# Kernel tuning notes

Hardware: AMD Instinct MI355X
Metric: run time of the kernel (lower is better)

The kernel has to match this reference:

```python
import jax, jax.numpy as jnp
import numpy as np
import math

# Mamba2Simple(d_model=192, d_state=128, d_conv=4, expand=4, headdim=32, chunk_size=256)
D_MODEL = 192
D_STATE = 128
D_CONV = 4
EXPAND = 4
HEADDIM = 32
D_INNER = EXPAND * D_MODEL                      # 768
NHEADS = D_INNER // HEADDIM                     # 24
CONV_DIM = D_INNER + 2 * D_STATE                # 1024 (ngroups=1)
D_IN_PROJ = 2 * D_INNER + 2 * D_STATE + NHEADS  # 1816
SEQ_PAD = 256                                   # forward pads dim-2 to 256
NUM_CLASS = 100
FEATURE_DIM = HEADDIM * D_STATE                 # 4096, classifier input


def make_pe(max_len, d_model):
    # TemporalPositionalEncoding buffer (sin/cos), added over the T axis.
    position = np.arange(max_len)[:, None].astype(np.float32)
    div_term = np.exp(np.arange(0, d_model, 2).astype(np.float32) * -(math.log(10000.0) / d_model))
    pe = np.zeros((max_len, d_model), np.float32)
    pe[:, 0::2] = np.sin(position * div_term)
    pe[:, 1::2] = np.cos(position * div_term)
    return jnp.asarray(pe)  # (max_len, d_model)


def setup_inputs() -> dict:
    key = jax.random.key(0)
    ks = jax.random.split(key, 8)
    B, T, S, D = 16, 8, 129, D_MODEL
    inputs = jax.random.normal(ks[0], (B, T, S, D), jnp.float32)
    in_proj_w = jax.random.normal(ks[1], (D_IN_PROJ, D_MODEL), jnp.float32) / np.sqrt(D_MODEL)
    conv_w = jax.random.normal(ks[2], (CONV_DIM, D_CONV), jnp.float32) / np.sqrt(D_CONV)
    conv_b = jax.random.normal(ks[3], (CONV_DIM,), jnp.float32) * 0.1
    # dt_bias = softplus^{-1}(dt) with dt ~ U[1e-3, 0.1] (Mamba2 init convention)
    dt0 = jax.random.uniform(ks[4], (NHEADS,), jnp.float32, 1e-3, 0.1)
    dt_bias = jnp.log(jnp.expm1(dt0))
    A_log = jnp.log(jax.random.uniform(ks[5], (NHEADS,), jnp.float32, 1.0, 16.0))
    cls_w = jax.random.normal(ks[6], (NUM_CLASS, FEATURE_DIM), jnp.float32) / np.sqrt(FEATURE_DIM)
    cls_b = jnp.zeros((NUM_CLASS,), jnp.float32)
    return dict(inputs=inputs, in_proj_w=in_proj_w, conv_w=conv_w, conv_b=conv_b,
                dt_bias=dt_bias, A_log=A_log, cls_w=cls_w, cls_b=cls_b)


def _mamba_final_state(u, in_proj_w, conv_w, conv_b, dt_bias, A_log):
    # u: (B, L, D_MODEL). Only the SSM final state is consumed downstream
    # (the module does `_, final_state = self.mamba(...)`), so the z / C / D /
    # RMSNormGated / out_proj branches, which never touch the state, are skipped.
    B_, L, _ = u.shape
    W = in_proj_w[D_INNER:, :]                              # rows for xBC (1024) + dt (24)
    proj = jnp.einsum('bld,ed->ble', u, W)                  # (B, L, 1048)
    xBC, dt_raw = proj[..., :CONV_DIM], proj[..., CONV_DIM:]
    # causal depthwise conv1d (kernel D_CONV) + SiLU
    xpad = jnp.pad(xBC, ((0, 0), (D_CONV - 1, 0), (0, 0)))
    conv = conv_b + sum(xpad[:, k:k + L, :] * conv_w[:, k] for k in range(D_CONV))
    xBC = jax.nn.silu(conv)
    x = xBC[..., :D_INNER].reshape(B_, L, NHEADS, HEADDIM)  # (B, L, H, P)
    Bmat = xBC[..., D_INNER:D_INNER + D_STATE]              # (B, L, N), ngroups=1
    dt = jax.nn.softplus(dt_raw + dt_bias)                  # (B, L, H)
    A = -jnp.exp(A_log)                                     # (H,), negative
    # Recurrence: h_t = exp(dt_t*A) * h_{t-1} + dt_t * x_t (outer) B_t.
    # Final state in closed form via exclusive suffix products of exp(dt*A):
    logdA = dt * A                                          # (B, L, H), <= 0
    csum = jnp.cumsum(logdA, axis=1)
    suffix = jnp.exp(csum[:, -1:, :] - csum)                # prod_{s>t} exp(dt_s*A)
    w = suffix * dt                                         # (B, L, H)
    return jnp.einsum('blh,blhp,bln->bhpn', w, x, Bmat)     # (B, H, P, N)


def reference(inputs, in_proj_w, conv_w, conv_b, dt_bias, A_log, cls_w, cls_b):
    # Dropout layers are identity in eval mode.
    B_, T, S, D = inputs.shape
    x = inputs[:, :, 1:, :]                                 # drop first sub-seq element
    pad = SEQ_PAD - x.shape[2]
    if pad > 0:
        x = jnp.pad(x, ((0, 0), (0, 0), (0, pad), (0, 0)))
    pe = make_pe(T, D)
    x = x + pe[None, :, None, :]                            # pe broadcast over batch & sub-seq
    preds = []
    for t in range(T):                                      # module re-runs scan on each suffix
        xt = x[:, t:, :, :].reshape(B_, -1, D)              # (B, (T-t)*256, D)
        h = _mamba_final_state(xt, in_proj_w, conv_w, conv_b, dt_bias, A_log)
        agg = h.sum(axis=1).reshape(B_, FEATURE_DIM)        # sum over heads -> (B, P*N)
        preds.append(agg @ cls_w.T + cls_b)
    return jnp.stack(preds, axis=1)                         # (B, T, NUM_CLASS)
```

## Files before the change

### kernel.cpp

```cpp
#include <hip/hip_runtime.h>
#include <math.h>

#define BATCH 16
#define TWIN 8
#define SEQIN 129
#define DMODEL 192
#define GLEN 2048
#define NH 24
#define HD 32
#define DS 128
#define NCC 896
#define MTOT (BATCH*GLEN)
#define NVALID (BATCH*TWIN*128)
#define PADK 104

typedef __attribute__((ext_vector_type(8))) short bf16x8;
typedef __attribute__((ext_vector_type(4))) float f32x4;

__device__ __forceinline__ float softplus_f(float x){
  return x > 20.f ? x : log1pf(expf(x));
}
__device__ __forceinline__ float silu_f(float x){
  return x / (1.f + __expf(-x));
}
__device__ __forceinline__ unsigned short tobf16(float f){
  union { float f; unsigned u; } v; v.f = f;
  unsigned r = v.u + 0x7FFF + ((v.u >> 16) & 1);
  return (unsigned short)(r >> 16);
}
__device__ __forceinline__ float frombf16(unsigned short u){
  union { unsigned u; float f; } v; v.u = ((unsigned)u) << 16; return v.f;
}
__device__ __forceinline__ bf16x8 pack8(float4 a, float4 b){
  bf16x8 r;
  r[0]=(short)tobf16(a.x); r[1]=(short)tobf16(a.y);
  r[2]=(short)tobf16(a.z); r[3]=(short)tobf16(a.w);
  r[4]=(short)tobf16(b.x); r[5]=(short)tobf16(b.y);
  r[6]=(short)tobf16(b.z); r[7]=(short)tobf16(b.w);
  return r;
}

__global__ __launch_bounds__(256) void k_build(const float* __restrict__ in,
    const float* __restrict__ inw, unsigned short* __restrict__ inh,
    unsigned short* __restrict__ wh, float* __restrict__ ptab,
    float* __restrict__ dtraw){
  __shared__ float smem[2048];
  int bx = blockIdx.x;
  int tid = threadIdx.x;
  if (bx < 768){
    int idx = (bx*256 + tid)*16;
    int v = idx / DMODEL;
    int d = idx - v*DMODEL;
    int bt = v >> 7, s = v & 127;
    const float* src = in + ((size_t)bt*SEQIN + s + 1)*DMODEL + d;
    float4 a0 = *(const float4*)src;
    float4 a1 = *(const float4*)(src+4);
    float4 a2 = *(const float4*)(src+8);
    float4 a3 = *(const float4*)(src+12);
    *(bf16x8*)&inh[idx]   = pack8(a0, a1);
    *(bf16x8*)&inh[idx+8] = pack8(a2, a3);
  } else if (bx < 852){
    int idx = ((bx-768)*256 + tid)*8;
    const float* src = inw + (size_t)768*DMODEL + idx;
    float4 a = *(const float4*)src;
    float4 b = *(const float4*)(src+4);
    *(bf16x8*)&wh[idx] = pack8(a, b);
  } else if (bx < 916){
    float* pe = smem;
    int pb = bx - 852;
    int t = pb >> 3, eslice = pb & 7;
    if (tid < DMODEL){
      int d = tid;
      float div = expf(-(float)(d & ~1) * (logf(10000.f)/(float)DMODEL));
      float ang = (float)t * div;
      pe[d] = (d & 1) ? cosf(ang) : sinf(ang);
    }
    __syncthreads();
    int e0 = eslice*115;
    int e1 = min(920, e0 + 115);
    for (int e = e0 + tid; e < e1; e += 256){
      int row = (e < 896) ? (768 + e) : (1792 + (e - 896));
      const float* wr = inw + (size_t)row*DMODEL;
      float s = 0.f;
      #pragma unroll 4
      for (int d = 0; d < DMODEL; d++)
        s += pe[d] * wr[d];
      ptab[t*920 + e] = s;
    }
  } else {
    float* As = smem;
    float* Bs = smem + 1024;
    int idx = bx - 916;
    int m0 = idx*64;
    int bt = m0 >> 7, srow = m0 & 127;
    int ty = tid >> 4, tx = tid & 15;
    int lr = tid >> 2, lq = tid & 3;
    float acc[4][4] = {};
    for (int k0 = 0; k0 < DMODEL; k0 += 16){
      float4 av = *(const float4*)(in + ((size_t)bt*SEQIN + srow + 1 + lr)*DMODEL + k0 + lq*4);
      As[(lq*4+0)*64+lr] = av.x; As[(lq*4+1)*64+lr] = av.y;
      As[(lq*4+2)*64+lr] = av.z; As[(lq*4+3)*64+lr] = av.w;
      float4 bv = make_float4(0.f,0.f,0.f,0.f);
      if (lr < NH) bv = *(const float4*)(inw + (size_t)(1792+lr)*DMODEL + k0 + lq*4);
      Bs[(lq*4+0)*64+lr] = bv.x; Bs[(lq*4+1)*64+lr] = bv.y;
      Bs[(lq*4+2)*64+lr] = bv.z; Bs[(lq*4+3)*64+lr] = bv.w;
      __syncthreads();
      #pragma unroll
      for (int kk = 0; kk < 16; kk++){
        float4 a = *(const float4*)&As[kk*64 + ty*4];
        float4 bq = *(const float4*)&Bs[kk*64 + tx*4];
        float avr[4] = {a.x, a.y, a.z, a.w};
        float bvr[4] = {bq.x, bq.y, bq.z, bq.w};
        #pragma unroll
        for (int i=0;i<4;i++)
          #pragma unroll
          for (int j=0;j<4;j++)
            acc[i][j] += avr[i]*bvr[j];
      }
      __syncthreads();
    }
    #pragma unroll
    for (int i=0;i<4;i++){
      int m = m0 + ty*4 + i;
      #pragma unroll
      for (int j=0;j<4;j++){
        int n = tx*4 + j;
        if (n < NH) dtraw[(size_t)m*NH + n] = acc[i][j];
      }
    }
  }
}

__global__ __launch_bounds__(256) void k_gemmall(const unsigned short* __restrict__ inh,
    const unsigned short* __restrict__ wh, const float* __restrict__ ptab,
    const float* __restrict__ dtraw, const float* __restrict__ dt_bias,
    const float* __restrict__ A_log, unsigned short* __restrict__ projh,
    float* __restrict__ wbuf, float* __restrict__ wsum){
  __shared__ char smem[53248];
  int bx = blockIdx.x;
  int tid = threadIdx.x;
  if (bx < 896){
    unsigned short* As = (unsigned short*)smem;
    unsigned short* Bs = As + 128*PADK;
    int mt = bx & 127;
    int n0 = (bx >> 7)*128;
    int t = mt & 7;
    size_t msrc = (size_t)mt*128;
    size_t mdst = (size_t)(mt >> 3)*GLEN + (size_t)t*256;
    int wid = tid >> 6, lane = tid & 63;
    int wm = (wid >> 1)*64, wn = (wid & 1)*64;
    int quad = lane >> 4, lm = lane & 15;
    int sr = tid >> 2, sq = tid & 3;
    f32x4 acc[4][4];
    #pragma unroll
    for (int i=0;i<4;i++)
      #pragma unroll
      for (int j=0;j<4;j++) acc[i][j] = (f32x4){0.f,0.f,0.f,0.f};
    for (int k0 = 0; k0 < DMODEL; k0 += 96){
      #pragma unroll
      for (int kk = 0; kk < 96; kk += 32){
        #pragma unroll
        for (int half=0; half<2; half++){
          int r = sr + half*64;
          *(bf16x8*)&As[r*PADK + kk + sq*8] =
            *(const bf16x8*)&inh[(msrc + r)*DMODEL + k0 + kk + sq*8];
          *(bf16x8*)&Bs[r*PADK + kk + sq*8] =
            *(const bf16x8*)&wh[(size_t)(n0+r)*DMODEL + k0 + kk + sq*8];
        }
      }
      __syncthreads();
      #pragma unroll
      for (int kk = 0; kk < 3; kk++){
        bf16x8 aF[4], bF[4];
        #pragma unroll
        for (int i=0;i<4;i++){
          aF[i] = *(const bf16x8*)&As[(wm + i*16 + lm)*PADK + kk*32 + quad*8];
          bF[i] = *(const bf16x8*)&Bs[(wn + i*16 + lm)*PADK + kk*32 + quad*8];
        }
        #pragma unroll
        for (int i=0;i<4;i++)
          #pragma unroll
          for (int j=0;j<4;j++)
            acc[i][j] = __builtin_amdgcn_mfma_f32_16x16x32_bf16(aF[i], bF[j], acc[i][j], 0,0,0);
      }
      __syncthreads();
    }
    float ptn[4];
    #pragma unroll
    for (int j=0;j<4;j++) ptn[j] = ptab[t*920 + n0 + wn + lm + j*16];
    #pragma unroll
    for (int i=0;i<4;i++){
      #pragma unroll
      for (int r=0;r<4;r++){
        int m = wm + i*16 + quad*4 + r;
        unsigned short* dst = projh + (mdst + m)*NCC + n0 + wn + lm;
        #pragma unroll
        for (int j=0;j<4;j++)
          dst[j*16] = tobf16(acc[i][j][r] + ptn[j]);
      }
    }
    {
      int r = tid >> 5;
      int c4 = (tid & 31)*4;
      float4 pv = *(const float4*)&ptab[t*920 + n0 + c4];
      ushort4 v;
      v.x = tobf16(pv.x); v.y = tobf16(pv.y);
      v.z = tobf16(pv.z); v.w = tobf16(pv.w);
      *(ushort4*)&projh[(mdst + 128 + r)*NCC + n0 + c4] = v;
    }
  } else {
    float* wtot = (float*)smem;
    float* sred = (float*)smem + 4;
    int idx = bx - 896;
    int h = idx % NH, b = idx / NH;
    int lane = tid & 63, wid = tid >> 6;
    int tw = tid >> 5, q = tid & 31;
    float dtb = dt_bias[h];
    float negA = -expf(A_log[h]);
    float off = ptab[tw*920 + 896 + h] + dtb;
    float dtv[8], pre[8];
    float run = 0.f;
    if (q < 16){
      size_t rb = ((size_t)(b*TWIN + tw)*128 + q*8)*NH + h;
      #pragma unroll
      for (int i=0;i<8;i++){
        float dt = softplus_f(dtraw[rb + (size_t)i*NH] + off);
        run += dt * negA;
        dtv[i] = dt; pre[i] = run;
      }
    } else {
      float dt = softplus_f(off);
      #pragma unroll
      for (int i=0;i<8;i++){
        run += dt * negA;
        dtv[i] = dt; pre[i] = run;
      }
    }
    float v = run;
    #pragma unroll
    for (int o=1; o<64; o<<=1){
      float u = __shfl_up(v, o, 64);
      if (lane >= o) v += u;
    }
    if (lane == 63) wtot[wid] = v;
    __syncthreads();
    float base = 0.f, total = 0.f;
    #pragma unroll
    for (int w2=0; w2<4; w2++){
      float tv = wtot[w2];
      if (w2 < wid) base += tv;
      total += tv;
    }
    float excl = base + v - run;
    float ls = 0.f;
    size_t gb = (size_t)b*GLEN + tw*256 + q*8;
    #pragma unroll
    for (int i=0;i<8;i++){
      float w = expf(total - (excl + pre[i])) * dtv[i];
      if (q < 17) wbuf[(gb + i)*NH + h] = w;
      else ls += w;
    }
    sred[tid] = ls;
    __syncthreads();
    if (q == 17){
      float acc = ls;
      for (int r = 18; r < 32; r++) acc += sred[tw*32 + r];
      wsum[((size_t)b*TWIN + tw)*NH + h] = acc;
    }
  }
}

__global__ __launch_bounds__(256) void k_foldall(const unsigned short* __restrict__ projh,
    const float* __restrict__ conv_w, const float* __restrict__ conv_b,
    const float* __restrict__ wbuf, const float* __restrict__ ptab,
    const float* __restrict__ wsum, float* __restrict__ partial,
    float* __restrict__ cB, float* __restrict__ cbuf){
  __shared__ float smem[5440];
  int bx = blockIdx.x;
  int tid = threadIdx.x;
  if (bx < 512){
    int bt = bx >> 2, sub = bx & 3;
    int b = bt >> 3, t = bt & 7;
    int wave = tid >> 6, lane = tid & 63;
    int g0 = t*256 + sub*34;
    int wstart = wave*8 + (wave > 0 ? 1 : 0);
    int gw = g0 + wstart;
    size_t rbase = (size_t)b*GLEN;
    float* ybuf = smem;
    float cb[7][2], cw[7][2][4];
    #pragma unroll
    for (int k=0;k<7;k++){
      int c = 2*lane + 128*k;
      float2 tb = *(const float2*)&conv_b[c];
      cb[k][0]=tb.x; cb[k][1]=tb.y;
      float4 w0 = *(const float4*)&conv_w[c*4];
      float4 w1 = *(const float4*)&conv_w[(c+1)*4];
      cw[k][0][0]=w0.x; cw[k][0][1]=w0.y; cw[k][0][2]=w0.z; cw[k][0][3]=w0.w;
      cw[k][1][0]=w1.x; cw[k][1][1]=w1.y; cw[k][1][2]=w1.z; cw[k][1][3]=w1.w;
    }
    float h0[7][2], h1[7][2], h2[7][2];
    #pragma unroll
    for (int k=0;k<7;k++){
      h0[k][0]=h0[k][1]=h1[k][0]=h1[k][1]=h2[k][0]=h2[k][1]=0.f;
    }
    if (gw >= 3){
      if ((gw & 255) == 0){
        int tp = (gw >> 8) - 1;
        #pragma unroll
        for (int k=0;k<7;k++){
          int c = 2*lane + 128*k;
          float v0 = frombf16(tobf16(ptab[tp*920 + c]));
          float v1 = frombf16(tobf16(ptab[tp*920 + c + 1]));
          h0[k][0]=v0; h0[k][1]=v1;
          h1[k][0]=v0; h1[k][1]=v1;
          h2[k][0]=v0; h2[k][1]=v1;
        }
      } else {
        #pragma unroll
        for (int k=0;k<7;k++){
          int c = 2*lane + 128*k;
          ushort2 p0 = *(const ushort2*)&projh[(rbase+gw-3)*NCC + c];
          ushort2 p1 = *(const ushort2*)&projh[(rbase+gw-2)*NCC + c];
          ushort2 p2 = *(const ushort2*)&projh[(rbase+gw-1)*NCC + c];
          h0[k][0]=frombf16(p0.x); h0[k][1]=frombf16(p0.y);
          h1[k][0]=frombf16(p1.x); h1[k][1]=frombf16(p1.y);
          h2[k][0]=frombf16(p2.x); h2[k][1]=frombf16(p2.y);
        }
      }
    }
    #pragma unroll
    for (int i=0;i<9;i++){
      size_t row = rbase + gw + i;
      float wreg = (lane < NH) ? wbuf[row*NH + lane] : 0.f;
      float cur[7][2];
      #pragma unroll
      for (int k=0;k<7;k++){
        int c = 2*lane + 128*k;
        ushort2 pv = *(const ushort2*)&projh[row*NCC + c];
        cur[k][0]=frombf16(pv.x); cur[k][1]=frombf16(pv.y);
      }
      float py0=0.f, py1=0.f, b0v=0.f, b1v=0.f;
      #pragma unroll
      for (int k=0;k<7;k++){
        float a0 = cb[k][0] + h0[k][0]*cw[k][0][0] + h1[k][0]*cw[k][0][1]
                            + h2[k][0]*cw[k][0][2] + cur[k][0]*cw[k][0][3];
        float a1 = cb[k][1] + h0[k][1]*cw[k][1][0] + h1[k][1]*cw[k][1][1]
                            + h2[k][1]*cw[k][1][2] + cur[k][1]*cw[k][1][3];
        float s0 = silu_f(a0), s1 = silu_f(a1);
        if (k < 6){
          float wh_ = __shfl(wreg, (lane>>4) + 4*k, 64);
          py0 += wh_*s0; py1 += wh_*s1;
        } else { b0v = s0; b1v = s1; }
      }
      py0 += __shfl_xor(py0, 16, 64); py0 += __shfl_xor(py0, 32, 64);
      py1 += __shfl_xor(py1, 16, 64); py1 += __shfl_xor(py1, 32, 64);
      float* dst = ybuf + (wstart + i)*160;
      if (lane < 16) *(float2*)&dst[2*lane] = make_float2(py0, py1);
      *(float2*)&dst[32 + 2*lane] = make_float2(b0v, b1v);
      #pragma unroll
      for (int k=0;k<7;k++){
        h0[k][0]=h1[k][0]; h0[k][1]=h1[k][1];
        h1[k][0]=h2[k][0]; h1[k][1]=h2[k][1];
        h2[k][0]=cur[k][0]; h2[k][1]=cur[k][1];
      }
    }
    __syncthreads();
    int p0 = (tid >> 5)*4, n0 = (tid & 31)*4;
    float acc[4][4] = {};
    #pragma unroll 2
    for (int gi = 0; gi < 34; gi++){
      float4 yv = *(const float4*)&ybuf[gi*160 + p0];
      float4 bv = *(const float4*)&ybuf[gi*160 + 32 + n0];
      float ya[4] = {yv.x,yv.y,yv.z,yv.w};
      float ba[4] = {bv.x,bv.y,bv.z,bv.w};
      #pragma unroll
      for (int i=0;i<4;i++)
        #pragma unroll
        for (int j=0;j<4;j++)
          acc[i][j] += ya[i]*ba[j];
    }
    size_t pb = ((size_t)bt*4 + sub)*4096;
    #pragma unroll
    for (int i=0;i<4;i++)
      #pragma unroll
      for (int j=0;j<4;j++)
        partial[pb + (p0+i)*128 + n0+j] = acc[i][j];
  } else if (bx < 640){
    float* Xc = smem;
    float* Ws = smem + 896;
    int idx = bx - 512;
    int t = idx & 7, b = idx >> 3;
    for (int c = tid; c < NCC; c += 256){
      float4 w = *(const float4*)&conv_w[c*4];
      float sw = w.x + w.y + w.z + w.w;
      float a = conv_b[c] + frombf16(tobf16(ptab[t*920 + c])) * sw;
      Xc[c] = silu_f(a);
    }
    if (tid < NH) Ws[tid] = wsum[((size_t)b*TWIN + t)*NH + tid];
    __syncthreads();
    float* dst = cB + ((size_t)(b*TWIN + t))*160;
    if (tid < 32){
      float y = 0.f;
      #pragma unroll
      for (int h=0;h<NH;h++) y += Ws[h]*Xc[h*32 + tid];
      dst[tid] = y;
    } else if (tid < 160){
      dst[tid] = Xc[768 + tid - 32];
    }
  } else {
    float* xsw  = smem;
    float* xsg  = smem + 896;
    float* wv   = smem + 1792;
    float* bufw = smem + 1816;
    float* bufg = smem + 2296;
    int idx = bx - 640;
    int b = idx / 7, t = idx % 7 + 1;
    size_t rbase = (size_t)b*GLEN;
    int g0 = t*256;
    for (int gi=0; gi<3; gi++){
      int g = g0 + gi;
      if (tid < NH) wv[tid] = wbuf[(rbase+g)*NH + tid];
      for (int c = tid; c < NCC; c += 256){
        float aw = conv_b[c], ag = conv_b[c];
        #pragma unroll
        for (int k=0;k<4;k++){
          int gp = g - 3 + k;
          float pj = (gp >= g0) ? frombf16(projh[(rbase+gp)*NCC + c])
                                : frombf16(tobf16(ptab[(t-1)*920 + c]));
          float term = pj * conv_w[c*4+k];
          ag += term;
          if (gp >= g0) aw += term;
        }
        xsw[c] = silu_f(aw);
        xsg[c] = silu_f(ag);
      }
      __syncthreads();
      if (tid < 32){
        float yw = 0.f, yg = 0.f;
        #pragma unroll
        for (int h=0;h<NH;h++){ yw += wv[h]*xsw[h*32+tid]; yg += wv[h]*xsg[h*32+tid]; }
        bufw[gi*160 + tid] = yw;
        bufg[gi*160 + tid] = yg;
      } else if (tid < 160){
        bufw[gi*160 + tid] = xsw[768 + tid - 32];
        bufg[gi*160 + tid] = xsg[768 + tid - 32];
      }
      __syncthreads();
    }
    float* dst = cbuf + ((size_t)(b*TWIN + t))*960;
    for (int i = tid; i < 960; i += 256){
      int gi = i / 320, rem = i - gi*320;
      dst[i] = (rem < 160) ? bufw[gi*160 + rem] : bufg[gi*160 + rem - 160];
    }
  }
}

__global__ __launch_bounds__(256) void k_suffix(const float* __restrict__ partial,
    const float* __restrict__ cB, const float* __restrict__ cbuf,
    float* __restrict__ feat){
  int b = blockIdx.y;
  int e = blockIdx.x*256 + threadIdx.x;
  int p = e >> 7, n = e & 127;
  float s = 0.f;
  for (int t = TWIN-1; t >= 0; t--){
    int bt = b*TWIN + t;
    size_t pb = (size_t)bt*4*4096;
    s += partial[pb + e] + partial[pb + 4096 + e]
       + partial[pb + 2*4096 + e] + partial[pb + 3*4096 + e];
    const float* cb_ = cB + (size_t)bt*160;
    s += cb_[p] * cb_[32 + n];
    float f = s;
    if (t > 0){
      const float* cw_ = cbuf + (size_t)bt*960;
      #pragma unroll
      for (int gi=0; gi<3; gi++){
        const float* rw = cw_ + gi*320;
        f += rw[p]*rw[32+n] - rw[160+p]*rw[192+n];
      }
    }
    feat[(size_t)bt*4096 + e] = f;
  }
}

__global__ __launch_bounds__(256) void k_classifier(const float* __restrict__ feat,
    const float* __restrict__ cls_w, const float* __restrict__ cls_b,
    float* __restrict__ out){
  int bt0 = blockIdx.x*4;
  int k0  = blockIdx.y*8;
  int tid = threadIdx.x, wid = tid >> 6, lane = tid & 63;
  float acc[4][8] = {};
  int j0 = wid*1024;
  #pragma unroll
  for (int it = 0; it < 4; it++){
    int j = j0 + it*256 + lane*4;
    float4 f4[4], w4[8];
    #pragma unroll
    for (int i=0;i<4;i++) f4[i] = *(const float4*)(feat + (size_t)(bt0+i)*4096 + j);
    #pragma unroll
    for (int k=0;k<8;k++){
      int kr = k0 + k; kr = kr < 100 ? kr : 99;
      w4[k] = *(const float4*)(cls_w + (size_t)kr*4096 + j);
    }
    #pragma unroll
    for (int i=0;i<4;i++)
      #pragma unroll
      for (int k=0;k<8;k++)
        acc[i][k] += f4[i].x*w4[k].x + f4[i].y*w4[k].y
                   + f4[i].z*w4[k].z + f4[i].w*w4[k].w;
  }
  #pragma unroll
  for (int i=0;i<4;i++)
    #pragma unroll
    for (int k=0;k<8;k++)
      #pragma unroll
      for (int o=32; o>0; o>>=1)
        acc[i][k] += __shfl_down(acc[i][k], o, 64);
  __shared__ float part[4][32];
  if (lane == 0){
    #pragma unroll
    for (int i=0;i<4;i++)
      #pragma unroll
      for (int k=0;k<8;k++)
        part[wid][i*8+k] = acc[i][k];
  }
  __syncthreads();
  if (tid < 32){
    int i = tid >> 3, k = tid & 7;
    float s = part[0][tid] + part[1][tid] + part[2][tid] + part[3][tid];
    int kr = k0 + k;
    if (kr < 100) out[(size_t)(bt0+i)*100 + kr] = s + cls_b[kr];
  }
}

extern "C" void kernel_launch(void* const* d_in, const int* in_sizes, int n_in,
                              void* d_out, int out_size, void* d_ws, size_t ws_size,
                              hipStream_t stream){
  const float* inputs    = (const float*)d_in[0];
  const float* in_proj_w = (const float*)d_in[1];
  const float* conv_w    = (const float*)d_in[2];
  const float* conv_b    = (const float*)d_in[3];
  const float* dt_bias   = (const float*)d_in[4];
  const float* A_log     = (const float*)d_in[5];
  const float* cls_w     = (const float*)d_in[6];
  const float* cls_b     = (const float*)d_in[7];
  float* out = (float*)d_out;

  unsigned short* projh= (unsigned short*)d_ws;
  float* dtraw         = (float*)(projh + (size_t)MTOT*NCC);
  float* wbuf          = dtraw + (size_t)NVALID*NH;
  unsigned short* inh  = (unsigned short*)(wbuf + (size_t)MTOT*NH);
  unsigned short* wh   = inh + (size_t)NVALID*DMODEL;
  float* partial       = (float*)(wh + (size_t)NCC*DMODEL);
  float* feat          = partial + (size_t)512*4096;
  float* ptab          = feat + (size_t)128*4096;
  float* wsum          = ptab + (size_t)8*920;
  float* cB            = wsum + (size_t)128*NH;
  float* cbuf          = cB + (size_t)128*160;
  size_t need = (size_t)((char*)(cbuf + (size_t)128*960) - (char*)d_ws);
  if (ws_size < need) return;

  k_build      <<<1172, 256, 0, stream>>>(inputs, in_proj_w, inh, wh, ptab, dtraw);
  k_gemmall    <<<1280, 256, 0, stream>>>(inh, wh, ptab, dtraw, dt_bias, A_log,
                                          projh, wbuf, wsum);
  k_foldall    <<<752, 256, 0, stream>>>(projh, conv_w, conv_b, wbuf, ptab, wsum,
                                         partial, cB, cbuf);
  k_suffix     <<<dim3(16, BATCH), 256, 0, stream>>>(partial, cB, cbuf, feat);
  k_classifier <<<dim3(32, 13), 256, 0, stream>>>(feat, cls_w, cls_b, out);
}
```

Baseline: 153.3 us.

## Split fold blocks into 8 sub-chunks and preload conv rows into registers

The main fold stage now uses 8 sub-blocks of 17 rows per (batch, window) instead of 4 sub-blocks of 34. That doubles the block count and halves shared memory per block, which raises occupancy. Each wave loads all of its conv input rows, plus the halo, as packed bf16 pairs into registers up front, so loads are issued together instead of interleaved with compute. The GEMM epilogue also writes padding rows 253-255 with the positional-encoding value, which removes the special boundary branch. The cost is more partial-sum traffic and an 8-way reduction in the suffix kernel.

```diff
diff --git a/kernel.cpp b/kernel.cpp
--- a/kernel.cpp
+++ b/kernel.cpp
@@ -30,6 +30,12 @@
 }
 __device__ __forceinline__ float frombf16(unsigned short u){
   union { unsigned u; float f; } v; v.u = ((unsigned)u) << 16; return v.f;
+}
+__device__ __forceinline__ float bflo(unsigned u){
+  union { unsigned x; float f; } v; v.x = u << 16; return v.f;
+}
+__device__ __forceinline__ float bfhi(unsigned u){
+  union { unsigned x; float f; } v; v.x = u & 0xffff0000u; return v.f;
 }
 __device__ __forceinline__ bf16x8 pack8(float4 a, float4 b){
   bf16x8 r;
@@ -207,6 +213,8 @@
       v.x = tobf16(pv.x); v.y = tobf16(pv.y);
       v.z = tobf16(pv.z); v.w = tobf16(pv.w);
       *(ushort4*)&projh[(mdst + 128 + r)*NCC + n0 + c4] = v;
+      if (r < 3)
+        *(ushort4*)&projh[(mdst + 253 + r)*NCC + n0 + c4] = v;
     }
   } else {
     float* wtot = (float*)smem;
@@ -275,18 +283,38 @@
     const float* __restrict__ wbuf, const float* __restrict__ ptab,
     const float* __restrict__ wsum, float* __restrict__ partial,
     float* __restrict__ cB, float* __restrict__ cbuf){
-  __shared__ float smem[5440];
+  __shared__ float smem[2800];
   int bx = blockIdx.x;
   int tid = threadIdx.x;
-  if (bx < 512){
-    int bt = bx >> 2, sub = bx & 3;
+  if (bx < 1024){
+    int bt = bx >> 3, sub = bx & 7;
     int b = bt >> 3, t = bt & 7;
     int wave = tid >> 6, lane = tid & 63;
-    int g0 = t*256 + sub*34;
-    int wstart = wave*8 + (wave > 0 ? 1 : 0);
+    int g0 = t*256 + sub*17;
+    int wstart = wave*4;
     int gw = g0 + wstart;
+    int cnt = (wave == 3) ? 5 : 4;
     size_t rbase = (size_t)b*GLEN;
     float* ybuf = smem;
+    unsigned rows[8][7];
+    #pragma unroll
+    for (int j=0;j<8;j++){
+      if (j < cnt + 3){
+        int ridx = g0 + wstart - 3 + j;
+        if (ridx >= 0){
+          #pragma unroll
+          for (int k=0;k<7;k++)
+            rows[j][k] = *(const unsigned*)&projh[(rbase + ridx)*NCC + 2*lane + 128*k];
+        } else {
+          #pragma unroll
+          for (int k=0;k<7;k++) rows[j][k] = 0u;
+        }
+      }
+    }
+    float wreg[5];
+    #pragma unroll
+    for (int i=0;i<5;i++)
+      wreg[i] = (lane < NH && i < cnt) ? wbuf[(rbase + gw + i)*NH + lane] : 0.f;
     float cb[7][2], cw[7][2][4];
     #pragma unroll
     for (int k=0;k<7;k++){
@@ -298,77 +326,38 @@
       cw[k][0][0]=w0.x; cw[k][0][1]=w0.y; cw[k][0][2]=w0.z; cw[k][0][3]=w0.w;
       cw[k][1][0]=w1.x; cw[k][1][1]=w1.y; cw[k][1][2]=w1.z; cw[k][1][3]=w1.w;
     }
-    float h0[7][2], h1[7][2], h2[7][2];
-    #pragma unroll
-    for (int k=0;k<7;k++){
-      h0[k][0]=h0[k][1]=h1[k][0]=h1[k][1]=h2[k][0]=h2[k][1]=0.f;
-    }
-    if (gw >= 3){
-      if ((gw & 255) == 0){
-        int tp = (gw >> 8) - 1;
+    #pragma unroll
+    for (int i=0;i<5;i++){
+      if (i < cnt){
+        float py0=0.f, py1=0.f, b0v=0.f, b1v=0.f;
         #pragma unroll
         for (int k=0;k<7;k++){
-          int c = 2*lane + 128*k;
-          float v0 = frombf16(tobf16(ptab[tp*920 + c]));
-          float v1 = frombf16(tobf16(ptab[tp*920 + c + 1]));
-          h0[k][0]=v0; h0[k][1]=v1;
-          h1[k][0]=v0; h1[k][1]=v1;
-          h2[k][0]=v0; h2[k][1]=v1;
+          float a0 = cb[k][0] + bflo(rows[i][k])*cw[k][0][0]
+                              + bflo(rows[i+1][k])*cw[k][0][1]
+                              + bflo(rows[i+2][k])*cw[k][0][2]
+                              + bflo(rows[i+3][k])*cw[k][0][3];
+          float a1 = cb[k][1] + bfhi(rows[i][k])*cw[k][1][0]
+                              + bfhi(rows[i+1][k])*cw[k][1][1]
+                              + bfhi(rows[i+2][k])*cw[k][1][2]
+                              + bfhi(rows[i+3][k])*cw[k][1][3];
+          float s0 = silu_f(a0), s1 = silu_f(a1);
+          if (k < 6){
+            float wh_ = __shfl(wreg[i], (lane>>4) + 4*k, 64);
+            py0 += wh_*s0; py1 += wh_*s1;
+          } else { b0v = s0; b1v = s1; }
         }
-      } else {
-        #pragma unroll
-        for (int k=0;k<7;k++){
-          int c = 2*lane + 128*k;
-          ushort2 p0 = *(const ushort2*)&projh[(rbase+gw-3)*NCC + c];
-          ushort2 p1 = *(const ushort2*)&projh[(rbase+gw-2)*NCC + c];
-          ushort2 p2 = *(const ushort2*)&projh[(rbase+gw-1)*NCC + c];
-          h0[k][0]=frombf16(p0.x); h0[k][1]=frombf16(p0.y);
-          h1[k][0]=frombf16(p1.x); h1[k][1]=frombf16(p1.y);
-          h2[k][0]=frombf16(p2.x); h2[k][1]=frombf16(p2.y);
-        }
-      }
-    }
-    #pragma unroll
-    for (int i=0;i<9;i++){
-      size_t row = rbase + gw + i;
-      float wreg = (lane < NH) ? wbuf[row*NH + lane] : 0.f;
-      float cur[7][2];
-      #pragma unroll
-      for (int k=0;k<7;k++){
-        int c = 2*lane + 128*k;
-        ushort2 pv = *(const ushort2*)&projh[row*NCC + c];
-        cur[k][0]=frombf16(pv.x); cur[k][1]=frombf16(pv.y);
-      }
-      float py0=0.f, py1=0.f, b0v=0.f, b1v=0.f;
-      #pragma unroll
-      for (int k=0;k<7;k++){
-        float a0 = cb[k][0] + h0[k][0]*cw[k][0][0] + h1[k][0]*cw[k][0][1]
-                            + h2[k][0]*cw[k][0][2] + cur[k][0]*cw[k][0][3];
-        float a1 = cb[k][1] + h0[k][1]*cw[k][1][0] + h1[k][1]*cw[k][1][1]
-                            + h2[k][1]*cw[k][1][2] + cur[k][1]*cw[k][1][3];
-        float s0 = silu_f(a0), s1 = silu_f(a1);
-        if (k < 6){
-          float wh_ = __shfl(wreg, (lane>>4) + 4*k, 64);
-          py0 += wh_*s0; py1 += wh_*s1;
-        } else { b0v = s0; b1v = s1; }
-      }
-      py0 += __shfl_xor(py0, 16, 64); py0 += __shfl_xor(py0, 32, 64);
-      py1 += __shfl_xor(py1, 16, 64); py1 += __shfl_xor(py1, 32, 64);
-      float* dst = ybuf + (wstart + i)*160;
-      if (lane < 16) *(float2*)&dst[2*lane] = make_float2(py0, py1);
-      *(float2*)&dst[32 + 2*lane] = make_float2(b0v, b1v);
-      #pragma unroll
-      for (int k=0;k<7;k++){
-        h0[k][0]=h1[k][0]; h0[k][1]=h1[k][1];
-        h1[k][0]=h2[k][0]; h1[k][1]=h2[k][1];
-        h2[k][0]=cur[k][0]; h2[k][1]=cur[k][1];
+        py0 += __shfl_xor(py0, 16, 64); py0 += __shfl_xor(py0, 32, 64);
+        py1 += __shfl_xor(py1, 16, 64); py1 += __shfl_xor(py1, 32, 64);
+        float* dst = ybuf + (wstart + i)*160;
+        if (lane < 16) *(float2*)&dst[2*lane] = make_float2(py0, py1);
+        *(float2*)&dst[32 + 2*lane] = make_float2(b0v, b1v);
       }
     }
     __syncthreads();
     int p0 = (tid >> 5)*4, n0 = (tid & 31)*4;
     float acc[4][4] = {};
     #pragma unroll 2
-    for (int gi = 0; gi < 34; gi++){
+    for (int gi = 0; gi < 17; gi++){
       float4 yv = *(const float4*)&ybuf[gi*160 + p0];
       float4 bv = *(const float4*)&ybuf[gi*160 + 32 + n0];
       float ya[4] = {yv.x,yv.y,yv.z,yv.w};
@@ -379,16 +368,16 @@
         for (int j=0;j<4;j++)
           acc[i][j] += ya[i]*ba[j];
     }
-    size_t pb = ((size_t)bt*4 + sub)*4096;
+    size_t pb = ((size_t)bt*8 + sub)*4096;
     #pragma unroll
     for (int i=0;i<4;i++)
       #pragma unroll
       for (int j=0;j<4;j++)
         partial[pb + (p0+i)*128 + n0+j] = acc[i][j];
-  } else if (bx < 640){
+  } else if (bx < 1152){
     float* Xc = smem;
     float* Ws = smem + 896;
-    int idx = bx - 512;
+    int idx = bx - 1024;
     int t = idx & 7, b = idx >> 3;
     for (int c = tid; c < NCC; c += 256){
       float4 w = *(const float4*)&conv_w[c*4];
@@ -413,7 +402,7 @@
     float* wv   = smem + 1792;
     float* bufw = smem + 1816;
     float* bufg = smem + 2296;
-    int idx = bx - 640;
+    int idx = bx - 1152;
     int b = idx / 7, t = idx % 7 + 1;
     size_t rbase = (size_t)b*GLEN;
     int g0 = t*256;
@@ -464,9 +453,10 @@
   float s = 0.f;
   for (int t = TWIN-1; t >= 0; t--){
     int bt = b*TWIN + t;
-    size_t pb = (size_t)bt*4*4096;
-    s += partial[pb + e] + partial[pb + 4096 + e]
-       + partial[pb + 2*4096 + e] + partial[pb + 3*4096 + e];
+    size_t pb = (size_t)bt*8*4096;
+    #pragma unroll
+    for (int q=0;q<8;q++)
+      s += partial[pb + (size_t)q*4096 + e];
     const float* cb_ = cB + (size_t)bt*160;
     s += cb_[p] * cb_[32 + n];
     float f = s;
@@ -551,7 +541,7 @@
   unsigned short* inh  = (unsigned short*)(wbuf + (size_t)MTOT*NH);
   unsigned short* wh   = inh + (size_t)NVALID*DMODEL;
   float* partial       = (float*)(wh + (size_t)NCC*DMODEL);
-  float* feat          = partial + (size_t)512*4096;
+  float* feat          = partial + (size_t)1024*4096;
   float* ptab          = feat + (size_t)128*4096;
   float* wsum          = ptab + (size_t)8*920;
   float* cB            = wsum + (size_t)128*NH;
@@ -562,8 +552,8 @@
   k_build      <<<1172, 256, 0, stream>>>(inputs, in_proj_w, inh, wh, ptab, dtraw);
   k_gemmall    <<<1280, 256, 0, stream>>>(inh, wh, ptab, dtraw, dt_bias, A_log,
                                           projh, wbuf, wsum);
-  k_foldall    <<<752, 256, 0, stream>>>(projh, conv_w, conv_b, wbuf, ptab, wsum,
-                                         partial, cB, cbuf);
+  k_foldall    <<<1264, 256, 0, stream>>>(projh, conv_w, conv_b, wbuf, ptab, wsum,
+                                          partial, cB, cbuf);
   k_suffix     <<<dim3(16, BATCH), 256, 0, stream>>>(partial, cB, cbuf, feat);
   k_classifier <<<dim3(32, 13), 256, 0, stream>>>(feat, cls_w, cls_b, out);
 }
```

Result: no change. 152.3 us (-0.7%).

## Fuse depthwise conv and SiLU into GEMM epilogue, store compact activations

Applied to the files above, without the earlier changes.

The GEMM epilogue now stages each 128x128 output tile in shared memory together with halo rows, applies the causal depthwise conv and SiLU there, and writes bf16 activations to a compact per-window buffer of 136 rows instead of the full padded projection. A small side buffer keeps the first three raw projection rows per window for the boundary-correction path. The fold kernel then just loads the precomputed activations into LDS, reducing them with the dt weights before the outer product. This removes the conv and SiLU recomputation and padded-row traffic from the fold stage, at the cost of a heavier GEMM epilogue, an extra barrier, and a larger LDS footprint in the fold kernel that may lower occupancy.

```diff
diff --git a/kernel.cpp b/kernel.cpp
--- a/kernel.cpp
+++ b/kernel.cpp
@@ -13,6 +13,8 @@
 #define MTOT (BATCH*GLEN)
 #define NVALID (BATCH*TWIN*128)
 #define PADK 104
+#define PITCH 136
+#define XPITCH 928
 
 typedef __attribute__((ext_vector_type(8))) short bf16x8;
 typedef __attribute__((ext_vector_type(4))) float f32x4;
@@ -30,6 +32,12 @@
 }
 __device__ __forceinline__ float frombf16(unsigned short u){
   union { unsigned u; float f; } v; v.u = ((unsigned)u) << 16; return v.f;
+}
+__device__ __forceinline__ float bflo(unsigned u){
+  union { unsigned x; float f; } v; v.x = u << 16; return v.f;
+}
+__device__ __forceinline__ float bfhi(unsigned u){
+  union { unsigned x; float f; } v; v.x = u & 0xffff0000u; return v.f;
 }
 __device__ __forceinline__ bf16x8 pack8(float4 a, float4 b){
   bf16x8 r;
@@ -134,7 +142,10 @@
 __global__ __launch_bounds__(256) void k_gemmall(const unsigned short* __restrict__ inh,
     const unsigned short* __restrict__ wh, const float* __restrict__ ptab,
     const float* __restrict__ dtraw, const float* __restrict__ dt_bias,
-    const float* __restrict__ A_log, unsigned short* __restrict__ projh,
+    const float* __restrict__ A_log,
+    const float* __restrict__ conv_w, const float* __restrict__ conv_b,
+    unsigned short* __restrict__ sxh,
+    unsigned short* __restrict__ projb,
     float* __restrict__ wbuf, float* __restrict__ wsum){
   __shared__ char smem[53248];
   int bx = blockIdx.x;
@@ -146,7 +157,6 @@
     int n0 = (bx >> 7)*128;
     int t = mt & 7;
     size_t msrc = (size_t)mt*128;
-    size_t mdst = (size_t)(mt >> 3)*GLEN + (size_t)t*256;
     int wid = tid >> 6, lane = tid & 63;
     int wm = (wid >> 1)*64, wn = (wid & 1)*64;
     int quad = lane >> 4, lm = lane & 15;
@@ -185,6 +195,7 @@
       }
       __syncthreads();
     }
+    unsigned short* P = (unsigned short*)smem;
     float ptn[4];
     #pragma unroll
     for (int j=0;j<4;j++) ptn[j] = ptab[t*920 + n0 + wn + lm + j*16];
@@ -193,20 +204,44 @@
       #pragma unroll
       for (int r=0;r<4;r++){
         int m = wm + i*16 + quad*4 + r;
-        unsigned short* dst = projh + (mdst + m)*NCC + n0 + wn + lm;
         #pragma unroll
         for (int j=0;j<4;j++)
-          dst[j*16] = tobf16(acc[i][j][r] + ptn[j]);
-      }
-    }
+          P[(m+3)*PITCH + wn + lm + j*16] = tobf16(acc[i][j][r] + ptn[j]);
+      }
+    }
+    if (tid < 128){
+      int c = tid;
+      unsigned short pc = tobf16(ptab[t*920 + n0 + c]);
+      unsigned short hc = (t > 0) ? tobf16(ptab[(t-1)*920 + n0 + c]) : (unsigned short)0;
+      P[0*PITCH + c] = hc; P[1*PITCH + c] = hc; P[2*PITCH + c] = hc;
+      #pragma unroll
+      for (int r=131;r<139;r++) P[r*PITCH + c] = pc;
+    }
+    __syncthreads();
     {
-      int r = tid >> 5;
-      int c4 = (tid & 31)*4;
-      float4 pv = *(const float4*)&ptab[t*920 + n0 + c4];
-      ushort4 v;
-      v.x = tobf16(pv.x); v.y = tobf16(pv.y);
-      v.z = tobf16(pv.z); v.w = tobf16(pv.w);
-      *(ushort4*)&projh[(mdst + 128 + r)*NCC + n0 + c4] = v;
+      int cloc = 2*(tid & 63);
+      int cg = n0 + cloc;
+      float cbA = conv_b[cg], cbB = conv_b[cg+1];
+      float4 wA = *(const float4*)&conv_w[cg*4];
+      float4 wB = *(const float4*)&conv_w[(cg+1)*4];
+      int gq = (tid >> 6)*34;
+      size_t obase = (size_t)mt*136;
+      for (int k=0;k<34;k++){
+        int g = gq + k;
+        unsigned x0 = *(const unsigned*)&P[(g+0)*PITCH + cloc];
+        unsigned x1 = *(const unsigned*)&P[(g+1)*PITCH + cloc];
+        unsigned x2 = *(const unsigned*)&P[(g+2)*PITCH + cloc];
+        unsigned x3 = *(const unsigned*)&P[(g+3)*PITCH + cloc];
+        float a0 = cbA + bflo(x0)*wA.x + bflo(x1)*wA.y + bflo(x2)*wA.z + bflo(x3)*wA.w;
+        float a1 = cbB + bfhi(x0)*wB.x + bfhi(x1)*wB.y + bfhi(x2)*wB.z + bfhi(x3)*wB.w;
+        unsigned sv = (unsigned)tobf16(silu_f(a0)) | ((unsigned)tobf16(silu_f(a1)) << 16);
+        *(unsigned*)&sxh[(obase + g)*NCC + cg] = sv;
+      }
+    }
+    if (tid < 192){
+      int g = tid >> 6, c2 = 2*(tid & 63);
+      unsigned pv = *(const unsigned*)&P[(g+3)*PITCH + c2];
+      *(unsigned*)&projb[((size_t)mt*3 + g)*NCC + n0 + c2] = pv;
     }
   } else {
     float* wtot = (float*)smem;
@@ -270,109 +305,49 @@
   }
 }
 
-__global__ __launch_bounds__(256) void k_foldall(const unsigned short* __restrict__ projh,
+__global__ __launch_bounds__(256) void k_fold2(const unsigned short* __restrict__ sxh,
+    const unsigned short* __restrict__ projb,
     const float* __restrict__ conv_w, const float* __restrict__ conv_b,
     const float* __restrict__ wbuf, const float* __restrict__ ptab,
     const float* __restrict__ wsum, float* __restrict__ partial,
     float* __restrict__ cB, float* __restrict__ cbuf){
-  __shared__ float smem[5440];
+  __shared__ char smem[70720];
   int bx = blockIdx.x;
   int tid = threadIdx.x;
   if (bx < 512){
     int bt = bx >> 2, sub = bx & 3;
     int b = bt >> 3, t = bt & 7;
-    int wave = tid >> 6, lane = tid & 63;
-    int g0 = t*256 + sub*34;
-    int wstart = wave*8 + (wave > 0 ? 1 : 0);
-    int gw = g0 + wstart;
-    size_t rbase = (size_t)b*GLEN;
-    float* ybuf = smem;
-    float cb[7][2], cw[7][2][4];
-    #pragma unroll
-    for (int k=0;k<7;k++){
-      int c = 2*lane + 128*k;
-      float2 tb = *(const float2*)&conv_b[c];
-      cb[k][0]=tb.x; cb[k][1]=tb.y;
-      float4 w0 = *(const float4*)&conv_w[c*4];
-      float4 w1 = *(const float4*)&conv_w[(c+1)*4];
-      cw[k][0][0]=w0.x; cw[k][0][1]=w0.y; cw[k][0][2]=w0.z; cw[k][0][3]=w0.w;
-      cw[k][1][0]=w1.x; cw[k][1][1]=w1.y; cw[k][1][2]=w1.z; cw[k][1][3]=w1.w;
-    }
-    float h0[7][2], h1[7][2], h2[7][2];
-    #pragma unroll
-    for (int k=0;k<7;k++){
-      h0[k][0]=h0[k][1]=h1[k][0]=h1[k][1]=h2[k][0]=h2[k][1]=0.f;
-    }
-    if (gw >= 3){
-      if ((gw & 255) == 0){
-        int tp = (gw >> 8) - 1;
-        #pragma unroll
-        for (int k=0;k<7;k++){
-          int c = 2*lane + 128*k;
-          float v0 = frombf16(tobf16(ptab[tp*920 + c]));
-          float v1 = frombf16(tobf16(ptab[tp*920 + c + 1]));
-          h0[k][0]=v0; h0[k][1]=v1;
-          h1[k][0]=v0; h1[k][1]=v1;
-          h2[k][0]=v0; h2[k][1]=v1;
-        }
-      } else {
-        #pragma unroll
-        for (int k=0;k<7;k++){
-          int c = 2*lane + 128*k;
-          ushort2 p0 = *(const ushort2*)&projh[(rbase+gw-3)*NCC + c];
-          ushort2 p1 = *(const ushort2*)&projh[(rbase+gw-2)*NCC + c];
-          ushort2 p2 = *(const ushort2*)&projh[(rbase+gw-1)*NCC + c];
-          h0[k][0]=frombf16(p0.x); h0[k][1]=frombf16(p0.y);
-          h1[k][0]=frombf16(p1.x); h1[k][1]=frombf16(p1.y);
-          h2[k][0]=frombf16(p2.x); h2[k][1]=frombf16(p2.y);
-        }
-      }
-    }
-    #pragma unroll
-    for (int i=0;i<9;i++){
-      size_t row = rbase + gw + i;
-      float wreg = (lane < NH) ? wbuf[row*NH + lane] : 0.f;
-      float cur[7][2];
-      #pragma unroll
-      for (int k=0;k<7;k++){
-        int c = 2*lane + 128*k;
-        ushort2 pv = *(const ushort2*)&projh[row*NCC + c];
-        cur[k][0]=frombf16(pv.x); cur[k][1]=frombf16(pv.y);
-      }
-      float py0=0.f, py1=0.f, b0v=0.f, b1v=0.f;
-      #pragma unroll
-      for (int k=0;k<7;k++){
-        float a0 = cb[k][0] + h0[k][0]*cw[k][0][0] + h1[k][0]*cw[k][0][1]
-                            + h2[k][0]*cw[k][0][2] + cur[k][0]*cw[k][0][3];
-        float a1 = cb[k][1] + h0[k][1]*cw[k][1][0] + h1[k][1]*cw[k][1][1]
-                            + h2[k][1]*cw[k][1][2] + cur[k][1]*cw[k][1][3];
-        float s0 = silu_f(a0), s1 = silu_f(a1);
-        if (k < 6){
-          float wh_ = __shfl(wreg, (lane>>4) + 4*k, 64);
-          py0 += wh_*s0; py1 += wh_*s1;
-        } else { b0v = s0; b1v = s1; }
-      }
-      py0 += __shfl_xor(py0, 16, 64); py0 += __shfl_xor(py0, 32, 64);
-      py1 += __shfl_xor(py1, 16, 64); py1 += __shfl_xor(py1, 32, 64);
-      float* dst = ybuf + (wstart + i)*160;
-      if (lane < 16) *(float2*)&dst[2*lane] = make_float2(py0, py1);
-      *(float2*)&dst[32 + 2*lane] = make_float2(b0v, b1v);
-      #pragma unroll
-      for (int k=0;k<7;k++){
-        h0[k][0]=h1[k][0]; h0[k][1]=h1[k][1];
-        h1[k][0]=h2[k][0]; h1[k][1]=h2[k][1];
-        h2[k][0]=cur[k][0]; h2[k][1]=cur[k][1];
-      }
-    }
-    __syncthreads();
-    int p0 = (tid >> 5)*4, n0 = (tid & 31)*4;
+    int g0s = sub*34;
+    unsigned short* Xs = (unsigned short*)smem;
+    float* ys = (float*)(smem + 34*XPITCH*2);
+    float* ws = (float*)(smem + 34*XPITCH*2 + 34*32*4);
+    size_t srow = ((size_t)bt*136 + g0s)*NCC;
+    for (int i = tid; i < 34*448; i += 256){
+      int g = i / 448, w = i - g*448;
+      *(unsigned*)&Xs[g*XPITCH + 2*w] = *(const unsigned*)&sxh[srow + (size_t)g*NCC + 2*w];
+    }
+    size_t wrow = ((size_t)b*GLEN + t*256 + g0s)*NH;
+    for (int i = tid; i < 34*24; i += 256){
+      int g = i / 24, h = i - g*24;
+      ws[g*24 + h] = wbuf[wrow + (size_t)g*NH + h];
+    }
+    __syncthreads();
+    for (int i = tid; i < 34*32; i += 256){
+      int g = i >> 5, p = i & 31;
+      float y = 0.f;
+      #pragma unroll
+      for (int h = 0; h < NH; h++)
+        y += ws[g*24 + h]*frombf16(Xs[g*XPITCH + h*32 + p]);
+      ys[g*32 + p] = y;
+    }
+    __syncthreads();
+    int p0 = (tid >> 5)*4, nq = (tid & 31)*4;
     float acc[4][4] = {};
-    #pragma unroll 2
     for (int gi = 0; gi < 34; gi++){
-      float4 yv = *(const float4*)&ybuf[gi*160 + p0];
-      float4 bv = *(const float4*)&ybuf[gi*160 + 32 + n0];
-      float ya[4] = {yv.x,yv.y,yv.z,yv.w};
-      float ba[4] = {bv.x,bv.y,bv.z,bv.w};
+      float4 yv = *(const float4*)&ys[gi*32 + p0];
+      ushort4 bu = *(const ushort4*)&Xs[gi*XPITCH + 768 + nq];
+      float ya[4] = {yv.x, yv.y, yv.z, yv.w};
+      float ba[4] = {frombf16(bu.x), frombf16(bu.y), frombf16(bu.z), frombf16(bu.w)};
       #pragma unroll
       for (int i=0;i<4;i++)
         #pragma unroll
@@ -384,10 +359,10 @@
     for (int i=0;i<4;i++)
       #pragma unroll
       for (int j=0;j<4;j++)
-        partial[pb + (p0+i)*128 + n0+j] = acc[i][j];
+        partial[pb + (p0+i)*128 + nq+j] = acc[i][j];
   } else if (bx < 640){
-    float* Xc = smem;
-    float* Ws = smem + 896;
+    float* Xc = (float*)smem;
+    float* Ws = (float*)smem + 896;
     int idx = bx - 512;
     int t = idx & 7, b = idx >> 3;
     for (int c = tid; c < NCC; c += 256){
@@ -408,14 +383,15 @@
       dst[tid] = Xc[768 + tid - 32];
     }
   } else {
-    float* xsw  = smem;
-    float* xsg  = smem + 896;
-    float* wv   = smem + 1792;
-    float* bufw = smem + 1816;
-    float* bufg = smem + 2296;
+    float* xsw  = (float*)smem;
+    float* xsg  = (float*)smem + 896;
+    float* wv   = (float*)smem + 1792;
+    float* bufw = (float*)smem + 1816;
+    float* bufg = (float*)smem + 2296;
     int idx = bx - 640;
     int b = idx / 7, t = idx % 7 + 1;
     size_t rbase = (size_t)b*GLEN;
+    int bt = b*TWIN + t;
     int g0 = t*256;
     for (int gi=0; gi<3; gi++){
       int g = g0 + gi;
@@ -425,7 +401,7 @@
         #pragma unroll
         for (int k=0;k<4;k++){
           int gp = g - 3 + k;
-          float pj = (gp >= g0) ? frombf16(projh[(rbase+gp)*NCC + c])
+          float pj = (gp >= g0) ? frombf16(projb[((size_t)bt*3 + (gp - g0))*NCC + c])
                                 : frombf16(tobf16(ptab[(t-1)*920 + c]));
           float term = pj * conv_w[c*4+k];
           ag += term;
@@ -447,7 +423,7 @@
       }
       __syncthreads();
     }
-    float* dst = cbuf + ((size_t)(b*TWIN + t))*960;
+    float* dst = cbuf + ((size_t)bt)*960;
     for (int i = tid; i < 960; i += 256){
       int gi = i / 320, rem = i - gi*320;
       dst[i] = (rem < 160) ? bufw[gi*160 + rem] : bufg[gi*160 + rem - 160];
@@ -545,8 +521,9 @@
   const float* cls_b     = (const float*)d_in[7];
   float* out = (float*)d_out;
 
-  unsigned short* projh= (unsigned short*)d_ws;
-  float* dtraw         = (float*)(projh + (size_t)MTOT*NCC);
+  unsigned short* sxh  = (unsigned short*)d_ws;
+  unsigned short* projb= sxh + (size_t)128*136*NCC;
+  float* dtraw         = (float*)(projb + (size_t)128*3*NCC);
   float* wbuf          = dtraw + (size_t)NVALID*NH;
   unsigned short* inh  = (unsigned short*)(wbuf + (size_t)MTOT*NH);
   unsigned short* wh   = inh + (size_t)NVALID*DMODEL;
@@ -561,9 +538,9 @@
 
   k_build      <<<1172, 256, 0, stream>>>(inputs, in_proj_w, inh, wh, ptab, dtraw);
   k_gemmall    <<<1280, 256, 0, stream>>>(inh, wh, ptab, dtraw, dt_bias, A_log,
-                                          projh, wbuf, wsum);
-  k_foldall    <<<752, 256, 0, stream>>>(projh, conv_w, conv_b, wbuf, ptab, wsum,
-                                         partial, cB, cbuf);
+                                          conv_w, conv_b, sxh, projb, wbuf, wsum);
+  k_fold2      <<<752, 256, 0, stream>>>(sxh, projb, conv_w, conv_b, wbuf, ptab,
+                                         wsum, partial, cB, cbuf);
   k_suffix     <<<dim3(16, BATCH), 256, 0, stream>>>(partial, cB, cbuf, feat);
   k_classifier <<<dim3(32, 13), 256, 0, stream>>>(feat, cls_w, cls_b, out);
 }
```

Result: no change. 153.1 us (-0.1%).
